# Optimization experiments

Measured on AMD Instinct MI355X. Metric: run time of the kernel, lower is better.

## Reference

```python
import jax, jax.numpy as jnp
import numpy as np

IN_CH = 32
H = W = 512
NUM_CAMS = 4096
N_RAYS = 524288
HIDDEN = 128
ALPHA = 1e-4
# tensor_config = ['xy','xz','yz'] -> axis index pairs into t (x,y,z)
AXES = ((0, 1), (0, 2), (1, 2))


def grid_sample_border(plane, coords):
    """Bilinear grid_sample, padding_mode='border', align_corners=True.
    plane: (C,H,W); coords: (N,2) in [-1,1], coords[:,0]->W axis, coords[:,1]->H axis.
    Returns (N,C)."""
    C, Hh, Ww = plane.shape
    x = (coords[:, 0] + 1.0) * 0.5 * (Ww - 1)
    y = (coords[:, 1] + 1.0) * 0.5 * (Hh - 1)
    x0f = jnp.floor(x)
    y0f = jnp.floor(y)
    wx = (x - x0f)[None, :]
    wy = (y - y0f)[None, :]
    x0 = jnp.clip(x0f.astype(jnp.int32), 0, Ww - 1)
    x1 = jnp.clip(x0f.astype(jnp.int32) + 1, 0, Ww - 1)
    y0 = jnp.clip(y0f.astype(jnp.int32), 0, Hh - 1)
    y1 = jnp.clip(y0f.astype(jnp.int32) + 1, 0, Hh - 1)
    v00 = plane[:, y0, x0]  # (C,N)
    v01 = plane[:, y0, x1]
    v10 = plane[:, y1, x0]
    v11 = plane[:, y1, x1]
    out = (v00 * (1 - wx) * (1 - wy) + v01 * wx * (1 - wy)
           + v10 * (1 - wx) * wy + v11 * wx * wy)
    return out.T


def exp_so3(r):
    """Rodrigues: axis-angle (N,3) -> rotation matrices (N,3,3)."""
    theta = jnp.linalg.norm(r, axis=-1)[:, None, None]
    z = jnp.zeros_like(r[:, 0])
    K = jnp.stack([z, -r[:, 2], r[:, 1],
                   r[:, 2], z, -r[:, 0],
                   -r[:, 1], r[:, 0], z], axis=-1).reshape(-1, 3, 3)
    A = jnp.sin(theta) / (theta + 1e-10)
    B = (1.0 - jnp.cos(theta)) / (theta * theta + 1e-10)
    return jnp.eye(3, dtype=r.dtype) + A * K + B * (K @ K)


def setup_inputs() -> dict:
    key = jax.random.key(0)
    ks = jax.random.split(key, 12)
    cam_id = jax.random.randint(ks[0], (N_RAYS,), 0, NUM_CAMS, dtype=jnp.int32)
    t = jax.random.uniform(ks[1], (NUM_CAMS, 3), minval=-1.0, maxval=1.0, dtype=jnp.float32)
    plane_xy = jax.random.normal(ks[2], (IN_CH, H, W), dtype=jnp.float32)
    plane_xz = jax.random.normal(ks[3], (IN_CH, H, W), dtype=jnp.float32)
    plane_yz = jax.random.normal(ks[4], (IN_CH, H, W), dtype=jnp.float32)
    in_chs = IN_CH * 3
    # kaiming_normal_ init: std = sqrt(2/fan_in)
    w1 = jax.random.normal(ks[5], (in_chs, HIDDEN), dtype=jnp.float32) * np.sqrt(2.0 / in_chs)
    b1 = jax.random.normal(ks[6], (HIDDEN,), dtype=jnp.float32) * 0.01
    w2 = jax.random.normal(ks[7], (HIDDEN, HIDDEN), dtype=jnp.float32) * np.sqrt(2.0 / HIDDEN)
    b2 = jax.random.normal(ks[8], (HIDDEN,), dtype=jnp.float32) * 0.01
    w3 = jax.random.normal(ks[9], (HIDDEN, 3), dtype=jnp.float32) * np.sqrt(2.0 / HIDDEN)
    b3 = jax.random.normal(ks[10], (3,), dtype=jnp.float32) * 0.01
    top = jax.random.normal(ks[11], (NUM_CAMS, 3, 4), dtype=jnp.float32)
    bottom = jnp.tile(jnp.array([[[0.0, 0.0, 0.0, 1.0]]], dtype=jnp.float32), (NUM_CAMS, 1, 1))
    init_c2w = jnp.concatenate([top, bottom], axis=1)  # (NUM_CAMS,4,4)
    return {"cam_id": cam_id, "t": t, "plane_xy": plane_xy, "plane_xz": plane_xz,
            "plane_yz": plane_yz, "w1": w1, "b1": b1, "w2": w2, "b2": b2,
            "w3": w3, "b3": b3, "init_c2w": init_c2w}


def reference(cam_id, t, plane_xy, plane_xz, plane_yz, w1, b1, w2, b2, w3, b3, init_c2w):
    ts = t[cam_id]  # (N,3) per-ray translation
    coords_all = jax.lax.stop_gradient(ts)  # coords use t.data in the original
    codes = []
    for plane, (ax, ay) in zip((plane_xy, plane_xz, plane_yz), AXES):
        coords = jnp.stack([coords_all[:, ax], coords_all[:, ay]], axis=-1)
        codes.append(grid_sample_border(plane, coords))  # (N,IN_CH)
    codes = jnp.concatenate(codes, axis=-1)  # (N, 3*IN_CH)
    h = jax.nn.silu(codes @ w1 + b1)
    h = jax.nn.silu(h @ w2 + b2)
    rot = (h @ w3 + b3) * ALPHA  # (N,3) axis-angle
    R = exp_so3(rot)  # (N,3,3)
    c2w34 = jnp.concatenate([R, ts[:, :, None]], axis=-1)  # (N,3,4)
    bottom = jnp.broadcast_to(jnp.array([0.0, 0.0, 0.0, 1.0], dtype=c2w34.dtype),
                              (c2w34.shape[0], 1, 4))
    c2ws = jnp.concatenate([c2w34, bottom], axis=1)  # (N,4,4)
    return c2ws @ init_c2w[cam_id]
```

## Files before the change

### kernel.cpp

```cpp
#include <hip/hip_runtime.h>
#include <hip/hip_bf16.h>
#include <math.h>

#define IN_CH 32
#define HWDIM 512
#define HIDDEN 128
#define N_RAYS 524288
#define NUM_CAMS 4096
#define ALPHA 1e-4f

__global__ __launch_bounds__(128) void percam_kernel(
    const float* __restrict__ t,
    const float* __restrict__ pxy,
    const float* __restrict__ pxz,
    const float* __restrict__ pyz,
    const float* __restrict__ w1, const float* __restrict__ b1,
    const float* __restrict__ w2, const float* __restrict__ b2,
    const float* __restrict__ w3, const float* __restrict__ b3,
    const float* __restrict__ init_c2w,
    float* __restrict__ table)
{
    const int cam = blockIdx.x;
    const int tid = threadIdx.x;

    __shared__ float codes[96];
    __shared__ float h1s[HIDDEN];
    __shared__ float h2s[HIDDEN];
    __shared__ float rot[3];
    __shared__ float c2w[12];

    const float ts0 = t[cam * 3 + 0];
    const float ts1 = t[cam * 3 + 1];
    const float ts2 = t[cam * 3 + 2];

    if (tid < 96) {
        const int p = tid >> 5;
        const int c = tid & 31;
        const float* plane = (p == 0) ? pxy : ((p == 1) ? pxz : pyz);
        float cx, cy;
        if (p == 0)      { cx = ts0; cy = ts1; }
        else if (p == 1) { cx = ts0; cy = ts2; }
        else             { cx = ts1; cy = ts2; }

        const float x = (cx + 1.0f) * 0.5f * (float)(HWDIM - 1);
        const float y = (cy + 1.0f) * 0.5f * (float)(HWDIM - 1);
        const float x0f = floorf(x);
        const float y0f = floorf(y);
        const float wx = x - x0f;
        const float wy = y - y0f;
        int x0 = (int)x0f;
        int y0 = (int)y0f;
        int x1 = x0 + 1;
        int y1 = y0 + 1;
        x0 = min(max(x0, 0), HWDIM - 1);
        x1 = min(max(x1, 0), HWDIM - 1);
        y0 = min(max(y0, 0), HWDIM - 1);
        y1 = min(max(y1, 0), HWDIM - 1);

        const float* pc = plane + (size_t)c * HWDIM * HWDIM;
        const float v00 = pc[y0 * HWDIM + x0];
        const float v01 = pc[y0 * HWDIM + x1];
        const float v10 = pc[y1 * HWDIM + x0];
        const float v11 = pc[y1 * HWDIM + x1];

        codes[tid] = v00 * (1.0f - wx) * (1.0f - wy)
                   + v01 * wx          * (1.0f - wy)
                   + v10 * (1.0f - wx) * wy
                   + v11 * wx          * wy;
    }
    __syncthreads();

    {
        float acc = b1[tid];
        #pragma unroll 8
        for (int k = 0; k < 96; ++k) {
            acc += codes[k] * w1[k * HIDDEN + tid];
        }
        h1s[tid] = acc / (1.0f + expf(-acc));
    }
    __syncthreads();

    {
        float acc = b2[tid];
        #pragma unroll 8
        for (int k = 0; k < HIDDEN; ++k) {
            acc += h1s[k] * w2[k * HIDDEN + tid];
        }
        h2s[tid] = acc / (1.0f + expf(-acc));
    }
    __syncthreads();

    if (tid < 3) {
        float acc = b3[tid];
        #pragma unroll 8
        for (int k = 0; k < HIDDEN; ++k) {
            acc += h2s[k] * w3[k * 3 + tid];
        }
        rot[tid] = acc * ALPHA;
    }
    __syncthreads();

    if (tid == 0) {
        const float a = rot[0], b = rot[1], c = rot[2];
        const float th2 = a * a + b * b + c * c;
        const float th = sqrtf(th2);
        const float A = sinf(th) / (th + 1e-10f);
        const float B = (1.0f - cosf(th)) / (th * th + 1e-10f);
        c2w[0]  = 1.0f + B * (-(c * c + b * b));
        c2w[1]  = A * (-c) + B * (a * b);
        c2w[2]  = A * b + B * (a * c);
        c2w[3]  = ts0;
        c2w[4]  = A * c + B * (a * b);
        c2w[5]  = 1.0f + B * (-(c * c + a * a));
        c2w[6]  = A * (-a) + B * (b * c);
        c2w[7]  = ts1;
        c2w[8]  = A * (-b) + B * (a * c);
        c2w[9]  = A * a + B * (b * c);
        c2w[10] = 1.0f + B * (-(a * a + b * b));
        c2w[11] = ts2;
    }
    __syncthreads();

    if (tid < 16) {
        const int i = tid >> 2;
        const int j = tid & 3;
        const float* ic = init_c2w + (size_t)cam * 16;
        float v;
        if (i < 3) {
            v = c2w[i * 4 + 0] * ic[0 * 4 + j]
              + c2w[i * 4 + 1] * ic[1 * 4 + j]
              + c2w[i * 4 + 2] * ic[2 * 4 + j]
              + c2w[i * 4 + 3] * ic[3 * 4 + j];
        } else {
            v = ic[3 * 4 + j];
        }
        table[(size_t)cam * 16 + tid] = v;
    }
}

__global__ __launch_bounds__(256) void gather_kernel(
    const int* __restrict__ cam_id,
    const float4* __restrict__ table,
    float4* __restrict__ out)
{
    const int idx = blockIdx.x * blockDim.x + threadIdx.x;
    if (idx >= N_RAYS * 4) return;
    const int ray = idx >> 2;
    const int q = idx & 3;
    const int cid = cam_id[ray];
    out[idx] = table[cid * 4 + q];
}

extern "C" void kernel_launch(void* const* d_in, const int* in_sizes, int n_in,
                              void* d_out, int out_size, void* d_ws, size_t ws_size,
                              hipStream_t stream) {
    const int*   cam_id   = (const int*)  d_in[0];
    const float* t        = (const float*)d_in[1];
    const float* pxy      = (const float*)d_in[2];
    const float* pxz      = (const float*)d_in[3];
    const float* pyz      = (const float*)d_in[4];
    const float* w1       = (const float*)d_in[5];
    const float* b1       = (const float*)d_in[6];
    const float* w2       = (const float*)d_in[7];
    const float* b2       = (const float*)d_in[8];
    const float* w3       = (const float*)d_in[9];
    const float* b3       = (const float*)d_in[10];
    const float* init_c2w = (const float*)d_in[11];

    float* table = (float*)d_ws;

    percam_kernel<<<NUM_CAMS, 128, 0, stream>>>(
        t, pxy, pxz, pyz, w1, b1, w2, b2, w3, b3, init_c2w, table);

    const int total = N_RAYS * 4;
    gather_kernel<<<(total + 255) / 256, 256, 0, stream>>>(
        cam_id, (const float4*)table, (float4*)d_out);
}
```

Measured before the change: 47.73 us.

## Split sampling into own kernel and batch per-camera MLP on bf16 MFMA

```diff
diff --git a/kernel.cpp b/kernel.cpp
--- a/kernel.cpp
+++ b/kernel.cpp
@@ -2,139 +2,213 @@
 #include <hip/hip_bf16.h>
 #include <math.h>
 
-#define IN_CH 32
 #define HWDIM 512
 #define HIDDEN 128
 #define N_RAYS 524288
 #define NUM_CAMS 4096
 #define ALPHA 1e-4f
 
-__global__ __launch_bounds__(128) void percam_kernel(
+typedef __attribute__((ext_vector_type(4))) float f32x4;
+typedef __attribute__((ext_vector_type(8))) short bf16x8;
+
+__device__ __forceinline__ unsigned short f2bf(float f) {
+    union { float f; unsigned u; } v; v.f = f;
+    unsigned r = v.u + 0x7FFFu + ((v.u >> 16) & 1u);
+    return (unsigned short)(r >> 16);
+}
+__device__ __forceinline__ float bf2f(unsigned short s) {
+    union { unsigned u; float f; } v; v.u = ((unsigned)s) << 16;
+    return v.f;
+}
+
+__global__ __launch_bounds__(256) void sample_kernel(
     const float* __restrict__ t,
     const float* __restrict__ pxy,
     const float* __restrict__ pxz,
     const float* __restrict__ pyz,
+    unsigned short* __restrict__ codes)
+{
+    const int n = blockIdx.x * 256 + threadIdx.x;
+    const int cam = n / 96;
+    const int f = n - cam * 96;
+    const int p = f >> 5;
+    const int c = f & 31;
+
+    const float ts0 = t[cam * 3 + 0];
+    const float ts1 = t[cam * 3 + 1];
+    const float ts2 = t[cam * 3 + 2];
+
+    const float* plane;
+    float cx, cy;
+    if (p == 0)      { plane = pxy; cx = ts0; cy = ts1; }
+    else if (p == 1) { plane = pxz; cx = ts0; cy = ts2; }
+    else             { plane = pyz; cx = ts1; cy = ts2; }
+
+    const float x = (cx + 1.0f) * 0.5f * (float)(HWDIM - 1);
+    const float y = (cy + 1.0f) * 0.5f * (float)(HWDIM - 1);
+    const float x0f = floorf(x);
+    const float y0f = floorf(y);
+    const float wx = x - x0f;
+    const float wy = y - y0f;
+    const int x0 = min(max((int)x0f, 0), HWDIM - 1);
+    const int x1 = min(max((int)x0f + 1, 0), HWDIM - 1);
+    const int y0 = min(max((int)y0f, 0), HWDIM - 1);
+    const int y1 = min(max((int)y0f + 1, 0), HWDIM - 1);
+
+    const float* pc = plane + (size_t)c * (HWDIM * HWDIM);
+    const float v00 = pc[y0 * HWDIM + x0];
+    const float v01 = pc[y0 * HWDIM + x1];
+    const float v10 = pc[y1 * HWDIM + x0];
+    const float v11 = pc[y1 * HWDIM + x1];
+
+    const float val = v00 * (1.0f - wx) * (1.0f - wy)
+                    + v01 * wx          * (1.0f - wy)
+                    + v10 * (1.0f - wx) * wy
+                    + v11 * wx          * wy;
+    codes[n] = f2bf(val);
+}
+
+#define W1S 104
+#define W2S 136
+#define HS  136
+
+__global__ __launch_bounds__(256) void mlp_kernel(
+    const unsigned short* __restrict__ codes,
+    const float* __restrict__ t,
     const float* __restrict__ w1, const float* __restrict__ b1,
     const float* __restrict__ w2, const float* __restrict__ b2,
     const float* __restrict__ w3, const float* __restrict__ b3,
     const float* __restrict__ init_c2w,
     float* __restrict__ table)
 {
-    const int cam = blockIdx.x;
-    const int tid = threadIdx.x;
-
-    __shared__ float codes[96];
-    __shared__ float h1s[HIDDEN];
-    __shared__ float h2s[HIDDEN];
-    __shared__ float rot[3];
-    __shared__ float c2w[12];
-
-    const float ts0 = t[cam * 3 + 0];
-    const float ts1 = t[cam * 3 + 1];
-    const float ts2 = t[cam * 3 + 2];
-
-    if (tid < 96) {
-        const int p = tid >> 5;
-        const int c = tid & 31;
-        const float* plane = (p == 0) ? pxy : ((p == 1) ? pxz : pyz);
-        float cx, cy;
-        if (p == 0)      { cx = ts0; cy = ts1; }
-        else if (p == 1) { cx = ts0; cy = ts2; }
-        else             { cx = ts1; cy = ts2; }
-
-        const float x = (cx + 1.0f) * 0.5f * (float)(HWDIM - 1);
-        const float y = (cy + 1.0f) * 0.5f * (float)(HWDIM - 1);
-        const float x0f = floorf(x);
-        const float y0f = floorf(y);
-        const float wx = x - x0f;
-        const float wy = y - y0f;
-        int x0 = (int)x0f;
-        int y0 = (int)y0f;
-        int x1 = x0 + 1;
-        int y1 = y0 + 1;
-        x0 = min(max(x0, 0), HWDIM - 1);
-        x1 = min(max(x1, 0), HWDIM - 1);
-        y0 = min(max(y0, 0), HWDIM - 1);
-        y1 = min(max(y1, 0), HWDIM - 1);
-
-        const float* pc = plane + (size_t)c * HWDIM * HWDIM;
-        const float v00 = pc[y0 * HWDIM + x0];
-        const float v01 = pc[y0 * HWDIM + x1];
-        const float v10 = pc[y1 * HWDIM + x0];
-        const float v11 = pc[y1 * HWDIM + x1];
-
-        codes[tid] = v00 * (1.0f - wx) * (1.0f - wy)
-                   + v01 * wx          * (1.0f - wy)
-                   + v10 * (1.0f - wx) * wy
-                   + v11 * wx          * wy;
-    }
-    __syncthreads();
-
+    const int tid  = threadIdx.x;
+    const int lane = tid & 63;
+    const int wave = tid >> 6;
+    const int cam0 = blockIdx.x * 16;
+    const int ncol = lane & 15;
+    const int kgrp = lane >> 4;
+
+    __shared__ unsigned short w1t[128][W1S];
+    __shared__ unsigned short w2t[128][W2S];
+    __shared__ unsigned short h1t[16][HS];
+    __shared__ unsigned short h2t[16][HS];
+    __shared__ float b1s[128], b2s[128], w3s[384];
+    __shared__ float rotc[16][3];
+    __shared__ float c2ws[16][12];
+
+    for (int i = tid; i < 96 * 128; i += 256) {
+        const int k = i >> 7, n = i & 127;
+        w1t[n][k] = f2bf(w1[i]);
+    }
+    for (int i = tid; i < 128 * 128; i += 256) {
+        const int k = i >> 7, n = i & 127;
+        w2t[n][k] = f2bf(w2[i]);
+    }
+    if (tid < 128) { b1s[tid] = b1[tid]; b2s[tid] = b2[tid]; }
+    for (int i = tid; i < 384; i += 256) w3s[i] = w3[i];
+    __syncthreads();
+
+    const int nb0 = wave * 32 + ncol;
+    const int nb1 = nb0 + 16;
+
+    f32x4 acc0, acc1;
     {
-        float acc = b1[tid];
-        #pragma unroll 8
-        for (int k = 0; k < 96; ++k) {
-            acc += codes[k] * w1[k * HIDDEN + tid];
+        const float bv0 = b1s[nb0], bv1 = b1s[nb1];
+        acc0 = (f32x4){bv0, bv0, bv0, bv0};
+        acc1 = (f32x4){bv1, bv1, bv1, bv1};
+    }
+    const unsigned short* arow = codes + (size_t)(cam0 + ncol) * 96;
+    #pragma unroll
+    for (int k0 = 0; k0 < 96; k0 += 32) {
+        const bf16x8 a   = *reinterpret_cast<const bf16x8*>(arow + k0 + kgrp * 8);
+        const bf16x8 bb0 = *reinterpret_cast<const bf16x8*>(&w1t[nb0][k0 + kgrp * 8]);
+        const bf16x8 bb1 = *reinterpret_cast<const bf16x8*>(&w1t[nb1][k0 + kgrp * 8]);
+        acc0 = __builtin_amdgcn_mfma_f32_16x16x32_bf16(a, bb0, acc0, 0, 0, 0);
+        acc1 = __builtin_amdgcn_mfma_f32_16x16x32_bf16(a, bb1, acc1, 0, 0, 0);
+    }
+    #pragma unroll
+    for (int r = 0; r < 4; ++r) {
+        const int camr = kgrp * 4 + r;
+        const float v0 = acc0[r];
+        const float v1 = acc1[r];
+        h1t[camr][nb0] = f2bf(v0 / (1.0f + __expf(-v0)));
+        h1t[camr][nb1] = f2bf(v1 / (1.0f + __expf(-v1)));
+    }
+    __syncthreads();
+
+    {
+        const float bv0 = b2s[nb0], bv1 = b2s[nb1];
+        acc0 = (f32x4){bv0, bv0, bv0, bv0};
+        acc1 = (f32x4){bv1, bv1, bv1, bv1};
+    }
+    #pragma unroll
+    for (int k0 = 0; k0 < 128; k0 += 32) {
+        const bf16x8 a   = *reinterpret_cast<const bf16x8*>(&h1t[ncol][k0 + kgrp * 8]);
+        const bf16x8 bb0 = *reinterpret_cast<const bf16x8*>(&w2t[nb0][k0 + kgrp * 8]);
+        const bf16x8 bb1 = *reinterpret_cast<const bf16x8*>(&w2t[nb1][k0 + kgrp * 8]);
+        acc0 = __builtin_amdgcn_mfma_f32_16x16x32_bf16(a, bb0, acc0, 0, 0, 0);
+        acc1 = __builtin_amdgcn_mfma_f32_16x16x32_bf16(a, bb1, acc1, 0, 0, 0);
+    }
+    #pragma unroll
+    for (int r = 0; r < 4; ++r) {
+        const int camr = kgrp * 4 + r;
+        const float v0 = acc0[r];
+        const float v1 = acc1[r];
+        h2t[camr][nb0] = f2bf(v0 / (1.0f + __expf(-v0)));
+        h2t[camr][nb1] = f2bf(v1 / (1.0f + __expf(-v1)));
+    }
+    __syncthreads();
+
+    if (tid < 64) {
+        const int cam = tid >> 2, c = tid & 3;
+        if (c < 3) {
+            float acc = b3[c];
+            for (int k = 0; k < 128; ++k)
+                acc += bf2f(h2t[cam][k]) * w3s[k * 3 + c];
+            rotc[cam][c] = acc * ALPHA;
         }
-        h1s[tid] = acc / (1.0f + expf(-acc));
-    }
-    __syncthreads();
-
-    {
-        float acc = b2[tid];
-        #pragma unroll 8
-        for (int k = 0; k < HIDDEN; ++k) {
-            acc += h1s[k] * w2[k * HIDDEN + tid];
-        }
-        h2s[tid] = acc / (1.0f + expf(-acc));
-    }
-    __syncthreads();
-
-    if (tid < 3) {
-        float acc = b3[tid];
-        #pragma unroll 8
-        for (int k = 0; k < HIDDEN; ++k) {
-            acc += h2s[k] * w3[k * 3 + tid];
-        }
-        rot[tid] = acc * ALPHA;
-    }
-    __syncthreads();
-
-    if (tid == 0) {
-        const float a = rot[0], b = rot[1], c = rot[2];
+    }
+    __syncthreads();
+
+    if (tid < 16) {
+        const int cam = tid;
+        const float a = rotc[cam][0], b = rotc[cam][1], c = rotc[cam][2];
         const float th2 = a * a + b * b + c * c;
         const float th = sqrtf(th2);
         const float A = sinf(th) / (th + 1e-10f);
-        const float B = (1.0f - cosf(th)) / (th * th + 1e-10f);
-        c2w[0]  = 1.0f + B * (-(c * c + b * b));
-        c2w[1]  = A * (-c) + B * (a * b);
-        c2w[2]  = A * b + B * (a * c);
-        c2w[3]  = ts0;
-        c2w[4]  = A * c + B * (a * b);
-        c2w[5]  = 1.0f + B * (-(c * c + a * a));
-        c2w[6]  = A * (-a) + B * (b * c);
-        c2w[7]  = ts1;
-        c2w[8]  = A * (-b) + B * (a * c);
-        c2w[9]  = A * a + B * (b * c);
-        c2w[10] = 1.0f + B * (-(a * a + b * b));
-        c2w[11] = ts2;
-    }
-    __syncthreads();
-
-    if (tid < 16) {
-        const int i = tid >> 2;
-        const int j = tid & 3;
-        const float* ic = init_c2w + (size_t)cam * 16;
+        const float B = (1.0f - cosf(th)) / (th2 + 1e-10f);
+        const float ts0 = t[(cam0 + cam) * 3 + 0];
+        const float ts1 = t[(cam0 + cam) * 3 + 1];
+        const float ts2 = t[(cam0 + cam) * 3 + 2];
+        c2ws[cam][0]  = 1.0f + B * (-(c * c + b * b));
+        c2ws[cam][1]  = A * (-c) + B * (a * b);
+        c2ws[cam][2]  = A * b + B * (a * c);
+        c2ws[cam][3]  = ts0;
+        c2ws[cam][4]  = A * c + B * (a * b);
+        c2ws[cam][5]  = 1.0f + B * (-(c * c + a * a));
+        c2ws[cam][6]  = A * (-a) + B * (b * c);
+        c2ws[cam][7]  = ts1;
+        c2ws[cam][8]  = A * (-b) + B * (a * c);
+        c2ws[cam][9]  = A * a + B * (b * c);
+        c2ws[cam][10] = 1.0f + B * (-(a * a + b * b));
+        c2ws[cam][11] = ts2;
+    }
+    __syncthreads();
+
+    {
+        const int cam = tid >> 4, e = tid & 15, i = e >> 2, j = e & 3;
+        const float* ic = init_c2w + (size_t)(cam0 + cam) * 16;
         float v;
         if (i < 3) {
-            v = c2w[i * 4 + 0] * ic[0 * 4 + j]
-              + c2w[i * 4 + 1] * ic[1 * 4 + j]
-              + c2w[i * 4 + 2] * ic[2 * 4 + j]
-              + c2w[i * 4 + 3] * ic[3 * 4 + j];
+            const float* cw = c2ws[cam];
+            v = cw[i * 4 + 0] * ic[0 + j]
+              + cw[i * 4 + 1] * ic[4 + j]
+              + cw[i * 4 + 2] * ic[8 + j]
+              + cw[i * 4 + 3] * ic[12 + j];
         } else {
-            v = ic[3 * 4 + j];
+            v = ic[12 + j];
         }
-        table[(size_t)cam * 16 + tid] = v;
+        table[(size_t)cam0 * 16 + tid] = v;
     }
 }
 
@@ -168,9 +242,12 @@
     const float* init_c2w = (const float*)d_in[11];
 
     float* table = (float*)d_ws;
-
-    percam_kernel<<<NUM_CAMS, 128, 0, stream>>>(
-        t, pxy, pxz, pyz, w1, b1, w2, b2, w3, b3, init_c2w, table);
+    unsigned short* codes = (unsigned short*)((char*)d_ws + NUM_CAMS * 16 * 4);
+
+    sample_kernel<<<(NUM_CAMS * 96) / 256, 256, 0, stream>>>(t, pxy, pxz, pyz, codes);
+
+    mlp_kernel<<<NUM_CAMS / 16, 256, 0, stream>>>(
+        codes, t, w1, b1, w2, b2, w3, b3, init_c2w, table);
 
     const int total = N_RAYS * 4;
     gather_kernel<<<(total + 255) / 256, 256, 0, stream>>>(
```

Result: faster. 42.46 us (-11.0%).
